# Optimization experiments

Hardware: AMD Instinct MI355X
Metric: run time of the kernel (lower is better)

The kernel has to match this reference:

```python
import jax, jax.numpy as jnp
import numpy as np

TOP_K = 2

def setup_inputs() -> dict:
    key = jax.random.key(0)
    ks = jax.random.split(key, 5)
    N, D, E, H, O = 2048, 1024, 16, 2048, 1024
    s_in = 1.0 / np.sqrt(D)
    s_h = 1.0 / np.sqrt(H)
    return {
        "z": jax.random.normal(ks[0], (N, D), dtype=jnp.float32),
        "router_w": jax.random.normal(ks[1], (E, D), dtype=jnp.float32) * s_in,
        "router_b": jnp.zeros((E,), dtype=jnp.float32),
        "w1": jax.random.normal(ks[2], (E, H, D), dtype=jnp.float32) * s_in,
        "b1": jnp.zeros((E, H), dtype=jnp.float32),
        "w2": jax.random.normal(ks[3], (E, O, H), dtype=jnp.float32) * s_h,
        "b2": jnp.zeros((E, O), dtype=jnp.float32),
    }

def reference(z, router_w, router_b, w1, b1, w2, b2):
    # Router: softmax over experts, then top-k with renormalized weights
    logits = z @ router_w.T + router_b                      # [N, E]
    probs = jax.nn.softmax(logits, axis=-1)                 # [N, E]
    topk_prob, topk_idx = jax.lax.top_k(probs, TOP_K)       # [N, K]
    topk_prob = topk_prob / topk_prob.sum(axis=-1, keepdims=True)

    # Dense all-expert MLP (faithful to original mix(): every expert on every token)
    h = jax.nn.gelu(jnp.einsum('nd,ehd->neh', z, w1) + b1, approximate=False)  # [N, E, H]
    expert_out = jnp.einsum('neh,eoh->neo', h, w2) + b2                        # [N, E, O]

    # Gather top-k expert outputs and combine with routing weights
    picked = jnp.take_along_axis(expert_out, topk_idx[:, :, None], axis=1)     # [N, K, O]
    return (picked * topk_prob[:, :, None]).sum(axis=1)                        # [N, O]
```

## Files before the change

### kernel.cpp

```cpp
#include <hip/hip_runtime.h>
#include <hip/hip_bf16.h>
#include <math.h>

#define N_TOK 2048
#define DIM   1024
#define NE    16
#define NH    2048
#define NO    1024

typedef __attribute__((ext_vector_type(8))) short short8;
typedef __attribute__((ext_vector_type(4))) float f32x4;

__device__ __forceinline__ unsigned short f2bf(float f) {
  union { float f; unsigned u; } v; v.f = f;
  unsigned r = v.u + 0x7FFFu + ((v.u >> 16) & 1u);
  return (unsigned short)(r >> 16);
}

__device__ __forceinline__ short8 pack8(float4 a, float4 b) {
  short8 r;
  r[0] = (short)f2bf(a.x); r[1] = (short)f2bf(a.y);
  r[2] = (short)f2bf(a.z); r[3] = (short)f2bf(a.w);
  r[4] = (short)f2bf(b.x); r[5] = (short)f2bf(b.y);
  r[6] = (short)f2bf(b.z); r[7] = (short)f2bf(b.w);
  return r;
}

__device__ __forceinline__ unsigned pkbf(float x, float y) {
  float2 f; f.x = x; f.y = y;
  __hip_bfloat162 b = __float22bfloat162_rn(f);
  unsigned u; __builtin_memcpy(&u, &b, 4);
  return u;
}
__device__ __forceinline__ short8 cvt8(float4 a, float4 b) {
  union { short8 s; unsigned u[4]; } r;
  r.u[0] = pkbf(a.x, a.y); r.u[1] = pkbf(a.z, a.w);
  r.u[2] = pkbf(b.x, b.y); r.u[3] = pkbf(b.z, b.w);
  return r.s;
}

__device__ __forceinline__ void glds16(const void* g, void* l) {
  __builtin_amdgcn_global_load_lds(
      (const __attribute__((address_space(1))) void*)g,
      (__attribute__((address_space(3))) void*)l, 16, 0, 0);
}

__device__ __forceinline__ void lds_barrier() {
  __builtin_amdgcn_s_waitcnt(0xC07F);
  __builtin_amdgcn_s_barrier();
}

__global__ __launch_bounds__(256) void router_kernel(
    const float* __restrict__ z, const float* __restrict__ rw,
    const float* __restrict__ rb, int* __restrict__ counts,
    int* __restrict__ list, float* __restrict__ tkw) {
  const int n = blockIdx.x;
  const int t = threadIdx.x;
  const int e = t >> 4, sub = t & 15;
  const float* zr = z + (size_t)n * DIM;
  const float* wr = rw + (size_t)e * DIM;
  double acc = 0.0;
#pragma unroll
  for (int i = 0; i < 16; ++i) {
    const int d = i * 64 + sub * 4;
    const float4 zv = *(const float4*)(zr + d);
    const float4 wv = *(const float4*)(wr + d);
    acc += (double)zv.x * wv.x + (double)zv.y * wv.y
         + (double)zv.z * wv.z + (double)zv.w * wv.w;
  }
  acc += __shfl_xor(acc, 8, 16);
  acc += __shfl_xor(acc, 4, 16);
  acc += __shfl_xor(acc, 2, 16);
  acc += __shfl_xor(acc, 1, 16);
  __shared__ double logits[NE];
  if (sub == 0) logits[e] = acc + (double)rb[e];
  __syncthreads();
  if (t == 0) {
    int i0 = -1, i1 = -1; double v0 = -1e300, v1 = -1e300;
    for (int i = 0; i < NE; ++i) {
      const double v = logits[i];
      if (v > v0) { v1 = v0; i1 = i0; v0 = v; i0 = i; }
      else if (v > v1) { v1 = v; i1 = i; }
    }
    const double w0 = 1.0 / (1.0 + exp(v1 - v0));
    tkw[n * 2 + 0] = (float)w0;
    tkw[n * 2 + 1] = (float)(1.0 - w0);
    const int p0 = atomicAdd(&counts[i0], 1); list[i0 * N_TOK + p0] = n * 2;
    const int p1 = atomicAdd(&counts[i1], 1); list[i1 * N_TOK + p1] = n * 2 + 1;
  }
}

__global__ __launch_bounds__(256) void convert_z_kernel(
    const float* __restrict__ z, unsigned short* __restrict__ zbf) {
  const int i = (blockIdx.x * 256 + threadIdx.x) * 8;
  const float4 a = *(const float4*)(z + i);
  const float4 b = *(const float4*)(z + i + 4);
  *(short8*)(zbf + i) = pack8(a, b);
}

#define BM 128
#define BN 128
#define BK 64
#define NNT1 (NH / BN)
#define NNT2 (NO / BN)
#define MT_LEVELS 8

__device__ __forceinline__ void decode_bid(int bid, int nent, int& mt, int& ent) {
  if (bid < 2 * nent) {
    mt = (bid >> 3) & 1;
    ent = (bid >> 4) * 8 + (bid & 7);
  } else {
    const int t2 = bid - 2 * nent;
    mt = 2 + t2 / nent;
    ent = t2 - (mt - 2) * nent;
  }
}

__global__ __launch_bounds__(256, 2) void gemm1_kernel(
    const unsigned short* __restrict__ zbf, const float* __restrict__ w1,
    const float* __restrict__ b1, const int* __restrict__ counts,
    const int* __restrict__ list, unsigned short* __restrict__ h) {
  int mt, ent;
  decode_bid(blockIdx.x, NE * NNT1, mt, ent);
  const int e  = ent >> 4;
  const int nt = ent & 15;
  const int ne = counts[e];
  if (mt * BM >= ne) return;
  const int t = threadIdx.x;

  __shared__ __align__(16) unsigned char As[BM * BK * 2];
  __shared__ __align__(16) unsigned char Bs[BN * BK * 4];
  __shared__ int ent_s[BM];
  if (t < BM) {
    const int idx = mt * BM + t;
    ent_s[t] = (idx < ne) ? list[e * N_TOK + idx] : -1;
  }
  __syncthreads();

  const int lane = t & 63, w = t >> 6;
  const unsigned short* aP[4];
  const float* bP[8];
  unsigned char *aL[4], *bL[8];
  {
    const int l3 = lane >> 3, c7 = lane & 7;
#pragma unroll
    for (int p = 0; p < 4; ++p) {
      const int CI = w + 4 * p;
      const int R = 8 * CI + l3;
      const int c = c7 ^ (R & 7);
      const int en = ent_s[R];
      aP[p] = zbf + (size_t)(en >= 0 ? (en >> 1) : 0) * DIM + c * 8;
      aL[p] = As + CI * 1024;
    }
    const int l4 = lane >> 4, c15 = lane & 15;
    const float* bbase = w1 + ((size_t)e * NH + (size_t)nt * BN) * DIM;
#pragma unroll
    for (int q = 0; q < 8; ++q) {
      const int CI = w + 4 * q;
      const int R = 4 * CI + l4;
      const int c = c15 ^ (R & 15);
      bP[q] = bbase + (size_t)R * DIM + c * 4;
      bL[q] = Bs + CI * 1024;
    }
  }

  const int wm = (w & 1) * 64, wn = (w >> 1) * 64;
  const int l15 = lane & 15, quad = lane >> 4;

  f32x4 acc[4][4];
#pragma unroll
  for (int i = 0; i < 4; ++i)
#pragma unroll
    for (int j = 0; j < 4; ++j) acc[i][j] = (f32x4){0.f, 0.f, 0.f, 0.f};

  for (int k0 = 0; k0 < DIM; k0 += BK) {
#pragma unroll
    for (int p = 0; p < 4; ++p) glds16(aP[p] + k0, aL[p]);
#pragma unroll
    for (int q = 0; q < 8; ++q) glds16(bP[q] + k0, bL[q]);
    __syncthreads();
#pragma unroll
    for (int kk = 0; kk < BK; kk += 32) {
      short8 af[4], bfr[4];
#pragma unroll
      for (int i = 0; i < 4; ++i) {
        const int R = wm + i * 16 + l15;
        const int c0 = (kk >> 3) + quad;
        af[i] = *(const short8*)(As + R * 128 + ((c0 ^ (R & 7)) << 4));
      }
#pragma unroll
      for (int j = 0; j < 4; ++j) {
        const int R = wn + j * 16 + l15;
        const int c0 = (kk >> 2) + 2 * quad;
        const float4 f0 = *(const float4*)(Bs + R * 256 + ((c0 ^ (R & 15)) << 4));
        const float4 f1 = *(const float4*)(Bs + R * 256 + (((c0 + 1) ^ (R & 15)) << 4));
        bfr[j] = cvt8(f0, f1);
      }
#pragma unroll
      for (int i = 0; i < 4; ++i)
#pragma unroll
        for (int j = 0; j < 4; ++j)
          acc[i][j] = __builtin_amdgcn_mfma_f32_16x16x32_bf16(af[i], bfr[j], acc[i][j], 0, 0, 0);
    }
    lds_barrier();
  }

  const int r4 = quad * 4;
#pragma unroll
  for (int i = 0; i < 4; ++i) {
#pragma unroll
    for (int reg = 0; reg < 4; ++reg) {
      const int row = wm + i * 16 + r4 + reg;
      const int en = ent_s[row];
      if (en < 0) continue;
      unsigned short* hrow = h + (size_t)en * NH;
#pragma unroll
      for (int j = 0; j < 4; ++j) {
        const int col = nt * BN + wn + j * 16 + l15;
        float v = acc[i][j][reg] + b1[e * NH + col];
        v = 0.5f * v * (1.0f + erff(v * 0.70710678118654752f));
        hrow[col] = f2bf(v);
      }
    }
  }
}

__global__ __launch_bounds__(256, 2) void gemm2_kernel(
    const unsigned short* __restrict__ h, const float* __restrict__ w2,
    const float* __restrict__ b2, const int* __restrict__ counts,
    const int* __restrict__ list, float* __restrict__ contrib) {
  int mt, ent;
  decode_bid(blockIdx.x, NE * NNT2, mt, ent);
  const int e  = ent >> 3;
  const int nt = ent & 7;
  const int ne = counts[e];
  if (mt * BM >= ne) return;
  const int t = threadIdx.x;

  __shared__ __align__(16) unsigned char As[BM * BK * 2];
  __shared__ __align__(16) unsigned char Bs[BN * BK * 4];
  __shared__ int ent_s[BM];
  if (t < BM) {
    const int idx = mt * BM + t;
    ent_s[t] = (idx < ne) ? list[e * N_TOK + idx] : -1;
  }
  __syncthreads();

  const int lane = t & 63, w = t >> 6;
  const unsigned short* aP[4];
  const float* bP[8];
  unsigned char *aL[4], *bL[8];
  {
    const int l3 = lane >> 3, c7 = lane & 7;
#pragma unroll
    for (int p = 0; p < 4; ++p) {
      const int CI = w + 4 * p;
      const int R = 8 * CI + l3;
      const int c = c7 ^ (R & 7);
      const int en = ent_s[R];
      aP[p] = h + (size_t)(en >= 0 ? en : 0) * NH + c * 8;
      aL[p] = As + CI * 1024;
    }
    const int l4 = lane >> 4, c15 = lane & 15;
    const float* bbase = w2 + ((size_t)e * NO + (size_t)nt * BN) * NH;
#pragma unroll
    for (int q = 0; q < 8; ++q) {
      const int CI = w + 4 * q;
      const int R = 4 * CI + l4;
      const int c = c15 ^ (R & 15);
      bP[q] = bbase + (size_t)R * NH + c * 4;
      bL[q] = Bs + CI * 1024;
    }
  }

  const int wm = (w & 1) * 64, wn = (w >> 1) * 64;
  const int l15 = lane & 15, quad = lane >> 4;

  f32x4 acc[4][4];
#pragma unroll
  for (int i = 0; i < 4; ++i)
#pragma unroll
    for (int j = 0; j < 4; ++j) acc[i][j] = (f32x4){0.f, 0.f, 0.f, 0.f};

  for (int k0 = 0; k0 < NH; k0 += BK) {
#pragma unroll
    for (int p = 0; p < 4; ++p) glds16(aP[p] + k0, aL[p]);
#pragma unroll
    for (int q = 0; q < 8; ++q) glds16(bP[q] + k0, bL[q]);
    __syncthreads();
#pragma unroll
    for (int kk = 0; kk < BK; kk += 32) {
      short8 af[4], bfr[4];
#pragma unroll
      for (int i = 0; i < 4; ++i) {
        const int R = wm + i * 16 + l15;
        const int c0 = (kk >> 3) + quad;
        af[i] = *(const short8*)(As + R * 128 + ((c0 ^ (R & 7)) << 4));
      }
#pragma unroll
      for (int j = 0; j < 4; ++j) {
        const int R = wn + j * 16 + l15;
        const int c0 = (kk >> 2) + 2 * quad;
        const float4 f0 = *(const float4*)(Bs + R * 256 + ((c0 ^ (R & 15)) << 4));
        const float4 f1 = *(const float4*)(Bs + R * 256 + (((c0 + 1) ^ (R & 15)) << 4));
        bfr[j] = cvt8(f0, f1);
      }
#pragma unroll
      for (int i = 0; i < 4; ++i)
#pragma unroll
        for (int j = 0; j < 4; ++j)
          acc[i][j] = __builtin_amdgcn_mfma_f32_16x16x32_bf16(af[i], bfr[j], acc[i][j], 0, 0, 0);
    }
    lds_barrier();
  }

  const int r4 = quad * 4;
#pragma unroll
  for (int i = 0; i < 4; ++i) {
#pragma unroll
    for (int reg = 0; reg < 4; ++reg) {
      const int row = wm + i * 16 + r4 + reg;
      const int en = ent_s[row];
      if (en < 0) continue;
      float* crow = contrib + (size_t)en * NO;
#pragma unroll
      for (int j = 0; j < 4; ++j) {
        const int col = nt * BN + wn + j * 16 + l15;
        crow[col] = acc[i][j][reg] + b2[e * NO + col];
      }
    }
  }
}

__global__ __launch_bounds__(256) void combine_kernel(
    const float* __restrict__ contrib, const float* __restrict__ tkw,
    float* __restrict__ out) {
  const int gid = blockIdx.x * 256 + threadIdx.x;
  const int n = gid >> 8;
  const int c = (gid & 255) * 4;
  const float w0 = tkw[n * 2], w1 = tkw[n * 2 + 1];
  const float4 a = *(const float4*)(contrib + (size_t)(n * 2) * NO + c);
  const float4 b = *(const float4*)(contrib + (size_t)(n * 2 + 1) * NO + c);
  float4 o;
  o.x = w0 * a.x + w1 * b.x; o.y = w0 * a.y + w1 * b.y;
  o.z = w0 * a.z + w1 * b.z; o.w = w0 * a.w + w1 * b.w;
  *(float4*)(out + (size_t)n * NO + c) = o;
}

extern "C" void kernel_launch(void* const* d_in, const int* in_sizes, int n_in,
                              void* d_out, int out_size, void* d_ws, size_t ws_size,
                              hipStream_t stream) {
  const float* z  = (const float*)d_in[0];
  const float* rw = (const float*)d_in[1];
  const float* rb = (const float*)d_in[2];
  const float* w1 = (const float*)d_in[3];
  const float* b1 = (const float*)d_in[4];
  const float* w2 = (const float*)d_in[5];
  const float* b2 = (const float*)d_in[6];
  float* out = (float*)d_out;

  char* ws = (char*)d_ws;
  int*   counts = (int*)ws;
  int*   list   = (int*)(ws + 256);
  float* tkw    = (float*)(ws + 256 + 131072);
  unsigned short* zbf = (unsigned short*)(ws + 262144);
  unsigned short* h = (unsigned short*)(ws + 262144 + 4194304);
  float* contrib = (float*)(ws + 262144 + 4194304 + 16777216);

  hipMemsetAsync(counts, 0, NE * sizeof(int), stream);
  convert_z_kernel<<<(N_TOK * DIM / 8) / 256, 256, 0, stream>>>(z, zbf);
  router_kernel<<<N_TOK, 256, 0, stream>>>(z, rw, rb, counts, list, tkw);
  gemm1_kernel<<<MT_LEVELS * NE * NNT1, 256, 0, stream>>>(zbf, w1, b1, counts, list, h);
  gemm2_kernel<<<MT_LEVELS * NE * NNT2, 256, 0, stream>>>(h, w2, b2, counts, list, contrib);
  combine_kernel<<<(N_TOK * (NO / 4)) / 256, 256, 0, stream>>>(contrib, tkw, out);
}
```

Baseline: 424.8 us.

## Double-buffer GEMM tiles and convert weights to bf16 before LDS store

```diff
diff --git a/kernel.cpp b/kernel.cpp
--- a/kernel.cpp
+++ b/kernel.cpp
@@ -43,11 +43,6 @@
   __builtin_amdgcn_global_load_lds(
       (const __attribute__((address_space(1))) void*)g,
       (__attribute__((address_space(3))) void*)l, 16, 0, 0);
-}
-
-__device__ __forceinline__ void lds_barrier() {
-  __builtin_amdgcn_s_waitcnt(0xC07F);
-  __builtin_amdgcn_s_barrier();
 }
 
 __global__ __launch_bounds__(256) void router_kernel(
@@ -104,6 +99,10 @@
 #define NNT1 (NH / BN)
 #define NNT2 (NO / BN)
 #define MT_LEVELS 8
+#define NT1 (DIM / BK)
+#define NT2 (NH / BK)
+#define ASZ (BM * BK * 2)
+#define BSZ (BN * BK * 2)
 
 __device__ __forceinline__ void decode_bid(int bid, int nent, int& mt, int& ent) {
   if (bid < 2 * nent) {
@@ -128,8 +127,8 @@
   if (mt * BM >= ne) return;
   const int t = threadIdx.x;
 
-  __shared__ __align__(16) unsigned char As[BM * BK * 2];
-  __shared__ __align__(16) unsigned char Bs[BN * BK * 4];
+  __shared__ __align__(16) unsigned char As[2 * ASZ];
+  __shared__ __align__(16) unsigned char Bs[2 * BSZ];
   __shared__ int ent_s[BM];
   if (t < BM) {
     const int idx = mt * BM + t;
@@ -139,8 +138,7 @@
 
   const int lane = t & 63, w = t >> 6;
   const unsigned short* aP[4];
-  const float* bP[8];
-  unsigned char *aL[4], *bL[8];
+  unsigned char* aL[4];
   {
     const int l3 = lane >> 3, c7 = lane & 7;
 #pragma unroll
@@ -152,17 +150,14 @@
       aP[p] = zbf + (size_t)(en >= 0 ? (en >> 1) : 0) * DIM + c * 8;
       aL[p] = As + CI * 1024;
     }
-    const int l4 = lane >> 4, c15 = lane & 15;
-    const float* bbase = w1 + ((size_t)e * NH + (size_t)nt * BN) * DIM;
-#pragma unroll
-    for (int q = 0; q < 8; ++q) {
-      const int CI = w + 4 * q;
-      const int R = 4 * CI + l4;
-      const int c = c15 ^ (R & 15);
-      bP[q] = bbase + (size_t)R * DIM + c * 4;
-      bL[q] = Bs + CI * 1024;
-    }
-  }
+  }
+  const int bR = w * 32 + (lane >> 1);
+  const int bh = lane & 1;
+  const float* bSrc = w1 + ((size_t)e * NH + (size_t)(nt * BN + bR)) * DIM + bh * 32;
+  unsigned char* bW[4];
+#pragma unroll
+  for (int j = 0; j < 4; ++j)
+    bW[j] = Bs + bR * 128 + (((bh * 4 + j) ^ (bR & 7)) << 4);
 
   const int wm = (w & 1) * 64, wn = (w >> 1) * 64;
   const int l15 = lane & 15, quad = lane >> 4;
@@ -173,28 +168,40 @@
 #pragma unroll
     for (int j = 0; j < 4; ++j) acc[i][j] = (f32x4){0.f, 0.f, 0.f, 0.f};
 
-  for (int k0 = 0; k0 < DIM; k0 += BK) {
-#pragma unroll
-    for (int p = 0; p < 4; ++p) glds16(aP[p] + k0, aL[p]);
-#pragma unroll
-    for (int q = 0; q < 8; ++q) glds16(bP[q] + k0, bL[q]);
-    __syncthreads();
+  float4 breg[8];
+#pragma unroll
+  for (int p = 0; p < 4; ++p) glds16(aP[p], aL[p]);
+#pragma unroll
+  for (int j = 0; j < 8; ++j) breg[j] = *(const float4*)(bSrc + j * 4);
+#pragma unroll
+  for (int j = 0; j < 4; ++j)
+    *(short8*)(bW[j]) = cvt8(breg[2 * j], breg[2 * j + 1]);
+  __syncthreads();
+
+  for (int kt = 0; kt < NT1; ++kt) {
+    const int cur = kt & 1, nxt = cur ^ 1;
+    const int k1 = (kt + 1) * BK;
+    if (kt + 1 < NT1) {
+#pragma unroll
+      for (int p = 0; p < 4; ++p) glds16(aP[p] + k1, aL[p] + nxt * ASZ);
+#pragma unroll
+      for (int j = 0; j < 8; ++j) breg[j] = *(const float4*)(bSrc + k1 + j * 4);
+    }
+    const unsigned char* Ac = As + cur * ASZ;
+    const unsigned char* Bc = Bs + cur * BSZ;
 #pragma unroll
     for (int kk = 0; kk < BK; kk += 32) {
       short8 af[4], bfr[4];
+      const int c0 = (kk >> 3) + quad;
 #pragma unroll
       for (int i = 0; i < 4; ++i) {
         const int R = wm + i * 16 + l15;
-        const int c0 = (kk >> 3) + quad;
-        af[i] = *(const short8*)(As + R * 128 + ((c0 ^ (R & 7)) << 4));
+        af[i] = *(const short8*)(Ac + R * 128 + ((c0 ^ (R & 7)) << 4));
       }
 #pragma unroll
       for (int j = 0; j < 4; ++j) {
         const int R = wn + j * 16 + l15;
-        const int c0 = (kk >> 2) + 2 * quad;
-        const float4 f0 = *(const float4*)(Bs + R * 256 + ((c0 ^ (R & 15)) << 4));
-        const float4 f1 = *(const float4*)(Bs + R * 256 + (((c0 + 1) ^ (R & 15)) << 4));
-        bfr[j] = cvt8(f0, f1);
+        bfr[j] = *(const short8*)(Bc + R * 128 + ((c0 ^ (R & 7)) << 4));
       }
 #pragma unroll
       for (int i = 0; i < 4; ++i)
@@ -202,7 +209,12 @@
         for (int j = 0; j < 4; ++j)
           acc[i][j] = __builtin_amdgcn_mfma_f32_16x16x32_bf16(af[i], bfr[j], acc[i][j], 0, 0, 0);
     }
-    lds_barrier();
+    if (kt + 1 < NT1) {
+#pragma unroll
+      for (int j = 0; j < 4; ++j)
+        *(short8*)(bW[j] + nxt * BSZ) = cvt8(breg[2 * j], breg[2 * j + 1]);
+      __syncthreads();
+    }
   }
 
   const int r4 = quad * 4;
@@ -237,8 +249,8 @@
   if (mt * BM >= ne) return;
   const int t = threadIdx.x;
 
-  __shared__ __align__(16) unsigned char As[BM * BK * 2];
-  __shared__ __align__(16) unsigned char Bs[BN * BK * 4];
+  __shared__ __align__(16) unsigned char As[2 * ASZ];
+  __shared__ __align__(16) unsigned char Bs[2 * BSZ];
   __shared__ int ent_s[BM];
   if (t < BM) {
     const int idx = mt * BM + t;
@@ -248,8 +260,7 @@
 
   const int lane = t & 63, w = t >> 6;
   const unsigned short* aP[4];
-  const float* bP[8];
-  unsigned char *aL[4], *bL[8];
+  unsigned char* aL[4];
   {
     const int l3 = lane >> 3, c7 = lane & 7;
 #pragma unroll
@@ -261,17 +272,14 @@
       aP[p] = h + (size_t)(en >= 0 ? en : 0) * NH + c * 8;
       aL[p] = As + CI * 1024;
     }
-    const int l4 = lane >> 4, c15 = lane & 15;
-    const float* bbase = w2 + ((size_t)e * NO + (size_t)nt * BN) * NH;
-#pragma unroll
-    for (int q = 0; q < 8; ++q) {
-      const int CI = w + 4 * q;
-      const int R = 4 * CI + l4;
-      const int c = c15 ^ (R & 15);
-      bP[q] = bbase + (size_t)R * NH + c * 4;
-      bL[q] = Bs + CI * 1024;
-    }
-  }
+  }
+  const int bR = w * 32 + (lane >> 1);
+  const int bh = lane & 1;
+  const float* bSrc = w2 + ((size_t)e * NO + (size_t)(nt * BN + bR)) * NH + bh * 32;
+  unsigned char* bW[4];
+#pragma unroll
+  for (int j = 0; j < 4; ++j)
+    bW[j] = Bs + bR * 128 + (((bh * 4 + j) ^ (bR & 7)) << 4);
 
   const int wm = (w & 1) * 64, wn = (w >> 1) * 64;
   const int l15 = lane & 15, quad = lane >> 4;
@@ -282,28 +290,40 @@
 #pragma unroll
     for (int j = 0; j < 4; ++j) acc[i][j] = (f32x4){0.f, 0.f, 0.f, 0.f};
 
-  for (int k0 = 0; k0 < NH; k0 += BK) {
-#pragma unroll
-    for (int p = 0; p < 4; ++p) glds16(aP[p] + k0, aL[p]);
-#pragma unroll
-    for (int q = 0; q < 8; ++q) glds16(bP[q] + k0, bL[q]);
-    __syncthreads();
+  float4 breg[8];
+#pragma unroll
+  for (int p = 0; p < 4; ++p) glds16(aP[p], aL[p]);
+#pragma unroll
+  for (int j = 0; j < 8; ++j) breg[j] = *(const float4*)(bSrc + j * 4);
+#pragma unroll
+  for (int j = 0; j < 4; ++j)
+    *(short8*)(bW[j]) = cvt8(breg[2 * j], breg[2 * j + 1]);
+  __syncthreads();
+
+  for (int kt = 0; kt < NT2; ++kt) {
+    const int cur = kt & 1, nxt = cur ^ 1;
+    const int k1 = (kt + 1) * BK;
+    if (kt + 1 < NT2) {
+#pragma unroll
+      for (int p = 0; p < 4; ++p) glds16(aP[p] + k1, aL[p] + nxt * ASZ);
+#pragma unroll
+      for (int j = 0; j < 8; ++j) breg[j] = *(const float4*)(bSrc + k1 + j * 4);
+    }
+    const unsigned char* Ac = As + cur * ASZ;
+    const unsigned char* Bc = Bs + cur * BSZ;
 #pragma unroll
     for (int kk = 0; kk < BK; kk += 32) {
       short8 af[4], bfr[4];
+      const int c0 = (kk >> 3) + quad;
 #pragma unroll
       for (int i = 0; i < 4; ++i) {
         const int R = wm + i * 16 + l15;
-        const int c0 = (kk >> 3) + quad;
-        af[i] = *(const short8*)(As + R * 128 + ((c0 ^ (R & 7)) << 4));
+        af[i] = *(const short8*)(Ac + R * 128 + ((c0 ^ (R & 7)) << 4));
       }
 #pragma unroll
       for (int j = 0; j < 4; ++j) {
         const int R = wn + j * 16 + l15;
-        const int c0 = (kk >> 2) + 2 * quad;
-        const float4 f0 = *(const float4*)(Bs + R * 256 + ((c0 ^ (R & 15)) << 4));
-        const float4 f1 = *(const float4*)(Bs + R * 256 + (((c0 + 1) ^ (R & 15)) << 4));
-        bfr[j] = cvt8(f0, f1);
+        bfr[j] = *(const short8*)(Bc + R * 128 + ((c0 ^ (R & 7)) << 4));
       }
 #pragma unroll
       for (int i = 0; i < 4; ++i)
@@ -311,7 +331,12 @@
         for (int j = 0; j < 4; ++j)
           acc[i][j] = __builtin_amdgcn_mfma_f32_16x16x32_bf16(af[i], bfr[j], acc[i][j], 0, 0, 0);
     }
-    lds_barrier();
+    if (kt + 1 < NT2) {
+#pragma unroll
+      for (int j = 0; j < 4; ++j)
+        *(short8*)(bW[j] + nxt * BSZ) = cvt8(breg[2 * j], breg[2 * j + 1]);
+      __syncthreads();
+    }
   }
 
   const int r4 = quad * 4;
```

New measurement: 500.6 us. 1.18x slower.

## Shrink MoE GEMM tiles, remap blocks per XCD, fuse combine via atomics

Applied to the files above, without the earlier changes.

```diff
diff --git a/kernel.cpp b/kernel.cpp
--- a/kernel.cpp
+++ b/kernel.cpp
@@ -98,38 +98,34 @@
   *(short8*)(zbf + i) = pack8(a, b);
 }
 
-#define BM 128
-#define BN 128
+#define BM 64
 #define BK 64
-#define NNT1 (NH / BN)
-#define NNT2 (NO / BN)
-#define MT_LEVELS 8
-
-__device__ __forceinline__ void decode_bid(int bid, int nent, int& mt, int& ent) {
-  if (bid < 2 * nent) {
-    mt = (bid >> 3) & 1;
-    ent = (bid >> 4) * 8 + (bid & 7);
-  } else {
-    const int t2 = bid - 2 * nent;
-    mt = 2 + t2 / nent;
-    ent = t2 - (mt - 2) * nent;
-  }
-}
-
-__global__ __launch_bounds__(256, 2) void gemm1_kernel(
+#define BN1 128
+#define BN2 64
+#define NT1 (DIM / BK)
+#define NT2 (NH / BK)
+#define MT_LEVELS 16
+#define GRID_G 4096
+
+__device__ __forceinline__ void decode_bid_xcd(int bid, int& mt, int& e, int& nt) {
+  const int slot = bid >> 3;
+  e = (bid & 7) + ((slot & 1) << 3);
+  mt = (slot >> 1) & 15;
+  nt = slot >> 5;
+}
+
+__global__ __launch_bounds__(256, 3) void gemm1_kernel(
     const unsigned short* __restrict__ zbf, const float* __restrict__ w1,
     const float* __restrict__ b1, const int* __restrict__ counts,
     const int* __restrict__ list, unsigned short* __restrict__ h) {
-  int mt, ent;
-  decode_bid(blockIdx.x, NE * NNT1, mt, ent);
-  const int e  = ent >> 4;
-  const int nt = ent & 15;
+  int mt, e, nt;
+  decode_bid_xcd(blockIdx.x, mt, e, nt);
   const int ne = counts[e];
   if (mt * BM >= ne) return;
   const int t = threadIdx.x;
 
   __shared__ __align__(16) unsigned char As[BM * BK * 2];
-  __shared__ __align__(16) unsigned char Bs[BN * BK * 4];
+  __shared__ __align__(16) unsigned char Bs[BN1 * BK * 4];
   __shared__ int ent_s[BM];
   if (t < BM) {
     const int idx = mt * BM + t;
@@ -138,13 +134,13 @@
   __syncthreads();
 
   const int lane = t & 63, w = t >> 6;
-  const unsigned short* aP[4];
+  const unsigned short* aP[2];
   const float* bP[8];
-  unsigned char *aL[4], *bL[8];
+  unsigned char *aL[2], *bL[8];
   {
     const int l3 = lane >> 3, c7 = lane & 7;
 #pragma unroll
-    for (int p = 0; p < 4; ++p) {
+    for (int p = 0; p < 2; ++p) {
       const int CI = w + 4 * p;
       const int R = 8 * CI + l3;
       const int c = c7 ^ (R & 7);
@@ -153,7 +149,7 @@
       aL[p] = As + CI * 1024;
     }
     const int l4 = lane >> 4, c15 = lane & 15;
-    const float* bbase = w1 + ((size_t)e * NH + (size_t)nt * BN) * DIM;
+    const float* bbase = w1 + ((size_t)e * NH + (size_t)nt * BN1) * DIM;
 #pragma unroll
     for (int q = 0; q < 8; ++q) {
       const int CI = w + 4 * q;
@@ -164,26 +160,26 @@
     }
   }
 
-  const int wm = (w & 1) * 64, wn = (w >> 1) * 64;
+  const int wm = (w & 1) * 32, wn = (w >> 1) * 64;
   const int l15 = lane & 15, quad = lane >> 4;
 
-  f32x4 acc[4][4];
-#pragma unroll
-  for (int i = 0; i < 4; ++i)
+  f32x4 acc[2][4];
+#pragma unroll
+  for (int i = 0; i < 2; ++i)
 #pragma unroll
     for (int j = 0; j < 4; ++j) acc[i][j] = (f32x4){0.f, 0.f, 0.f, 0.f};
 
   for (int k0 = 0; k0 < DIM; k0 += BK) {
 #pragma unroll
-    for (int p = 0; p < 4; ++p) glds16(aP[p] + k0, aL[p]);
+    for (int p = 0; p < 2; ++p) glds16(aP[p] + k0, aL[p]);
 #pragma unroll
     for (int q = 0; q < 8; ++q) glds16(bP[q] + k0, bL[q]);
     __syncthreads();
 #pragma unroll
     for (int kk = 0; kk < BK; kk += 32) {
-      short8 af[4], bfr[4];
-#pragma unroll
-      for (int i = 0; i < 4; ++i) {
+      short8 af[2], bfr[4];
+#pragma unroll
+      for (int i = 0; i < 2; ++i) {
         const int R = wm + i * 16 + l15;
         const int c0 = (kk >> 3) + quad;
         af[i] = *(const short8*)(As + R * 128 + ((c0 ^ (R & 7)) << 4));
@@ -197,7 +193,7 @@
         bfr[j] = cvt8(f0, f1);
       }
 #pragma unroll
-      for (int i = 0; i < 4; ++i)
+      for (int i = 0; i < 2; ++i)
 #pragma unroll
         for (int j = 0; j < 4; ++j)
           acc[i][j] = __builtin_amdgcn_mfma_f32_16x16x32_bf16(af[i], bfr[j], acc[i][j], 0, 0, 0);
@@ -207,7 +203,7 @@
 
   const int r4 = quad * 4;
 #pragma unroll
-  for (int i = 0; i < 4; ++i) {
+  for (int i = 0; i < 2; ++i) {
 #pragma unroll
     for (int reg = 0; reg < 4; ++reg) {
       const int row = wm + i * 16 + r4 + reg;
@@ -216,7 +212,7 @@
       unsigned short* hrow = h + (size_t)en * NH;
 #pragma unroll
       for (int j = 0; j < 4; ++j) {
-        const int col = nt * BN + wn + j * 16 + l15;
+        const int col = nt * BN1 + wn + j * 16 + l15;
         float v = acc[i][j][reg] + b1[e * NH + col];
         v = 0.5f * v * (1.0f + erff(v * 0.70710678118654752f));
         hrow[col] = f2bf(v);
@@ -225,20 +221,19 @@
   }
 }
 
-__global__ __launch_bounds__(256, 2) void gemm2_kernel(
+__global__ __launch_bounds__(256, 4) void gemm2_kernel(
     const unsigned short* __restrict__ h, const float* __restrict__ w2,
     const float* __restrict__ b2, const int* __restrict__ counts,
-    const int* __restrict__ list, float* __restrict__ contrib) {
-  int mt, ent;
-  decode_bid(blockIdx.x, NE * NNT2, mt, ent);
-  const int e  = ent >> 3;
-  const int nt = ent & 7;
+    const int* __restrict__ list, const float* __restrict__ tkw,
+    float* __restrict__ out) {
+  int mt, e, nt;
+  decode_bid_xcd(blockIdx.x, mt, e, nt);
   const int ne = counts[e];
   if (mt * BM >= ne) return;
   const int t = threadIdx.x;
 
   __shared__ __align__(16) unsigned char As[BM * BK * 2];
-  __shared__ __align__(16) unsigned char Bs[BN * BK * 4];
+  __shared__ __align__(16) unsigned char Bs[BN2 * BK * 4];
   __shared__ int ent_s[BM];
   if (t < BM) {
     const int idx = mt * BM + t;
@@ -247,13 +242,13 @@
   __syncthreads();
 
   const int lane = t & 63, w = t >> 6;
-  const unsigned short* aP[4];
-  const float* bP[8];
-  unsigned char *aL[4], *bL[8];
+  const unsigned short* aP[2];
+  const float* bP[4];
+  unsigned char *aL[2], *bL[4];
   {
     const int l3 = lane >> 3, c7 = lane & 7;
 #pragma unroll
-    for (int p = 0; p < 4; ++p) {
+    for (int p = 0; p < 2; ++p) {
       const int CI = w + 4 * p;
       const int R = 8 * CI + l3;
       const int c = c7 ^ (R & 7);
@@ -262,9 +257,9 @@
       aL[p] = As + CI * 1024;
     }
     const int l4 = lane >> 4, c15 = lane & 15;
-    const float* bbase = w2 + ((size_t)e * NO + (size_t)nt * BN) * NH;
-#pragma unroll
-    for (int q = 0; q < 8; ++q) {
+    const float* bbase = w2 + ((size_t)e * NO + (size_t)nt * BN2) * NH;
+#pragma unroll
+    for (int q = 0; q < 4; ++q) {
       const int CI = w + 4 * q;
       const int R = 4 * CI + l4;
       const int c = c15 ^ (R & 15);
@@ -273,32 +268,32 @@
     }
   }
 
-  const int wm = (w & 1) * 64, wn = (w >> 1) * 64;
+  const int wm = (w & 1) * 32, wn = (w >> 1) * 32;
   const int l15 = lane & 15, quad = lane >> 4;
 
-  f32x4 acc[4][4];
-#pragma unroll
-  for (int i = 0; i < 4; ++i)
-#pragma unroll
-    for (int j = 0; j < 4; ++j) acc[i][j] = (f32x4){0.f, 0.f, 0.f, 0.f};
+  f32x4 acc[2][2];
+#pragma unroll
+  for (int i = 0; i < 2; ++i)
+#pragma unroll
+    for (int j = 0; j < 2; ++j) acc[i][j] = (f32x4){0.f, 0.f, 0.f, 0.f};
 
   for (int k0 = 0; k0 < NH; k0 += BK) {
 #pragma unroll
-    for (int p = 0; p < 4; ++p) glds16(aP[p] + k0, aL[p]);
-#pragma unroll
-    for (int q = 0; q < 8; ++q) glds16(bP[q] + k0, bL[q]);
+    for (int p = 0; p < 2; ++p) glds16(aP[p] + k0, aL[p]);
+#pragma unroll
+    for (int q = 0; q < 4; ++q) glds16(bP[q] + k0, bL[q]);
     __syncthreads();
 #pragma unroll
     for (int kk = 0; kk < BK; kk += 32) {
-      short8 af[4], bfr[4];
-#pragma unroll
-      for (int i = 0; i < 4; ++i) {
+      short8 af[2], bfr[2];
+#pragma unroll
+      for (int i = 0; i < 2; ++i) {
         const int R = wm + i * 16 + l15;
         const int c0 = (kk >> 3) + quad;
         af[i] = *(const short8*)(As + R * 128 + ((c0 ^ (R & 7)) << 4));
       }
 #pragma unroll
-      for (int j = 0; j < 4; ++j) {
+      for (int j = 0; j < 2; ++j) {
         const int R = wn + j * 16 + l15;
         const int c0 = (kk >> 2) + 2 * quad;
         const float4 f0 = *(const float4*)(Bs + R * 256 + ((c0 ^ (R & 15)) << 4));
@@ -306,9 +301,9 @@
         bfr[j] = cvt8(f0, f1);
       }
 #pragma unroll
-      for (int i = 0; i < 4; ++i)
-#pragma unroll
-        for (int j = 0; j < 4; ++j)
+      for (int i = 0; i < 2; ++i)
+#pragma unroll
+        for (int j = 0; j < 2; ++j)
           acc[i][j] = __builtin_amdgcn_mfma_f32_16x16x32_bf16(af[i], bfr[j], acc[i][j], 0, 0, 0);
     }
     lds_barrier();
@@ -316,35 +311,21 @@
 
   const int r4 = quad * 4;
 #pragma unroll
-  for (int i = 0; i < 4; ++i) {
+  for (int i = 0; i < 2; ++i) {
 #pragma unroll
     for (int reg = 0; reg < 4; ++reg) {
       const int row = wm + i * 16 + r4 + reg;
       const int en = ent_s[row];
       if (en < 0) continue;
-      float* crow = contrib + (size_t)en * NO;
-#pragma unroll
-      for (int j = 0; j < 4; ++j) {
-        const int col = nt * BN + wn + j * 16 + l15;
-        crow[col] = acc[i][j][reg] + b2[e * NO + col];
-      }
-    }
-  }
-}
-
-__global__ __launch_bounds__(256) void combine_kernel(
-    const float* __restrict__ contrib, const float* __restrict__ tkw,
-    float* __restrict__ out) {
-  const int gid = blockIdx.x * 256 + threadIdx.x;
-  const int n = gid >> 8;
-  const int c = (gid & 255) * 4;
-  const float w0 = tkw[n * 2], w1 = tkw[n * 2 + 1];
-  const float4 a = *(const float4*)(contrib + (size_t)(n * 2) * NO + c);
-  const float4 b = *(const float4*)(contrib + (size_t)(n * 2 + 1) * NO + c);
-  float4 o;
-  o.x = w0 * a.x + w1 * b.x; o.y = w0 * a.y + w1 * b.y;
-  o.z = w0 * a.z + w1 * b.z; o.w = w0 * a.w + w1 * b.w;
-  *(float4*)(out + (size_t)n * NO + c) = o;
+      const float wgt = tkw[en];
+      float* orow = out + (size_t)(en >> 1) * NO;
+#pragma unroll
+      for (int j = 0; j < 2; ++j) {
+        const int col = nt * BN2 + wn + j * 16 + l15;
+        atomicAdd(&orow[col], wgt * (acc[i][j][reg] + b2[e * NO + col]));
+      }
+    }
+  }
 }
 
 extern "C" void kernel_launch(void* const* d_in, const int* in_sizes, int n_in,
@@ -365,12 +346,11 @@
   float* tkw    = (float*)(ws + 256 + 131072);
   unsigned short* zbf = (unsigned short*)(ws + 262144);
   unsigned short* h = (unsigned short*)(ws + 262144 + 4194304);
-  float* contrib = (float*)(ws + 262144 + 4194304 + 16777216);
 
   hipMemsetAsync(counts, 0, NE * sizeof(int), stream);
+  hipMemsetAsync(out, 0, (size_t)N_TOK * NO * sizeof(float), stream);
   convert_z_kernel<<<(N_TOK * DIM / 8) / 256, 256, 0, stream>>>(z, zbf);
   router_kernel<<<N_TOK, 256, 0, stream>>>(z, rw, rb, counts, list, tkw);
-  gemm1_kernel<<<MT_LEVELS * NE * NNT1, 256, 0, stream>>>(zbf, w1, b1, counts, list, h);
-  gemm2_kernel<<<MT_LEVELS * NE * NNT2, 256, 0, stream>>>(h, w2, b2, counts, list, contrib);
-  combine_kernel<<<(N_TOK * (NO / 4)) / 256, 256, 0, stream>>>(contrib, tkw, out);
-}
+  gemm1_kernel<<<GRID_G, 256, 0, stream>>>(zbf, w1, b1, counts, list, h);
+  gemm2_kernel<<<GRID_G, 256, 0, stream>>>(h, w2, b2, counts, list, tkw, out);
+}
```

Measured after the change: 478.5 us. 1.13x slower.

## Pre-convert expert weights to bf16 and use double-buffered direct-to-LDS GEMMs

Applied to the files above, without the earlier changes.

```diff
diff --git a/kernel.cpp b/kernel.cpp
--- a/kernel.cpp
+++ b/kernel.cpp
@@ -98,6 +98,233 @@
   *(short8*)(zbf + i) = pack8(a, b);
 }
 
+__global__ __launch_bounds__(256) void convert_w_kernel(
+    const float* __restrict__ src, unsigned short* __restrict__ dst) {
+  const size_t i = ((size_t)blockIdx.x * 256 + threadIdx.x) * 8;
+  const float4 a = *(const float4*)(src + i);
+  const float4 b = *(const float4*)(src + i + 4);
+  *(short8*)(dst + i) = cvt8(a, b);
+}
+
+#define BMF 128
+#define BKF 64
+#define ASZF (BMF * BKF * 2)
+
+__global__ __launch_bounds__(256, 2) void gemm1_fast(
+    const unsigned short* __restrict__ zbf, const unsigned short* __restrict__ w1b,
+    const float* __restrict__ b1, const int* __restrict__ counts,
+    const int* __restrict__ list, unsigned short* __restrict__ h) {
+  const int bid = blockIdx.x;
+  const int slot = bid >> 3;
+  const int e  = (bid & 7) | ((slot & 1) << 3);
+  const int mt = (slot >> 1) & 7;
+  const int nt = slot >> 4;
+  const int ne = counts[e];
+  if (mt * BMF >= ne) return;
+  const int t = threadIdx.x;
+
+  __shared__ __align__(16) unsigned char As[2 * ASZF];
+  __shared__ __align__(16) unsigned char Bs[2 * ASZF];
+  __shared__ int ent_s[BMF];
+  if (t < BMF) {
+    const int idx = mt * BMF + t;
+    ent_s[t] = (idx < ne) ? list[e * N_TOK + idx] : -1;
+  }
+  __syncthreads();
+
+  const int lane = t & 63, w = t >> 6;
+  const unsigned short *aP[4], *bP[4];
+  unsigned char *aL[4], *bL[4];
+  {
+    const int l3 = lane >> 3, c7 = lane & 7;
+    const unsigned short* bbase = w1b + ((size_t)e * NH + (size_t)nt * 128) * DIM;
+#pragma unroll
+    for (int p = 0; p < 4; ++p) {
+      const int CI = w + 4 * p;
+      const int R = 8 * CI + l3;
+      const int c = c7 ^ (R & 7);
+      const int en = ent_s[R];
+      aP[p] = zbf + (size_t)(en >= 0 ? (en >> 1) : 0) * DIM + c * 8;
+      aL[p] = As + CI * 1024;
+      bP[p] = bbase + (size_t)R * DIM + c * 8;
+      bL[p] = Bs + CI * 1024;
+    }
+  }
+  const int wm = (w & 1) * 64, wn = (w >> 1) * 64;
+  const int l15 = lane & 15, quad = lane >> 4;
+
+  f32x4 acc[4][4];
+#pragma unroll
+  for (int i = 0; i < 4; ++i)
+#pragma unroll
+    for (int j = 0; j < 4; ++j) acc[i][j] = (f32x4){0.f, 0.f, 0.f, 0.f};
+
+#pragma unroll
+  for (int p = 0; p < 4; ++p) { glds16(aP[p], aL[p]); glds16(bP[p], bL[p]); }
+  __syncthreads();
+
+  for (int kt = 0; kt < 16; ++kt) {
+    const int cur = kt & 1, nxt = cur ^ 1;
+    if (kt + 1 < 16) {
+      const int k1 = (kt + 1) * BKF;
+#pragma unroll
+      for (int p = 0; p < 4; ++p) {
+        glds16(aP[p] + k1, aL[p] + nxt * ASZF);
+        glds16(bP[p] + k1, bL[p] + nxt * ASZF);
+      }
+    }
+    const unsigned char* Ac = As + cur * ASZF;
+    const unsigned char* Bc = Bs + cur * ASZF;
+#pragma unroll
+    for (int kk = 0; kk < BKF; kk += 32) {
+      short8 af[4], bfr[4];
+      const int c0 = (kk >> 3) + quad;
+#pragma unroll
+      for (int i = 0; i < 4; ++i) {
+        const int Ra = wm + i * 16 + l15;
+        af[i] = *(const short8*)(Ac + Ra * 128 + ((c0 ^ (Ra & 7)) << 4));
+        const int Rb = wn + i * 16 + l15;
+        bfr[i] = *(const short8*)(Bc + Rb * 128 + ((c0 ^ (Rb & 7)) << 4));
+      }
+#pragma unroll
+      for (int i = 0; i < 4; ++i)
+#pragma unroll
+        for (int j = 0; j < 4; ++j)
+          acc[i][j] = __builtin_amdgcn_mfma_f32_16x16x32_bf16(af[i], bfr[j], acc[i][j], 0, 0, 0);
+    }
+    __syncthreads();
+  }
+
+  const int r4 = quad * 4;
+#pragma unroll
+  for (int i = 0; i < 4; ++i) {
+#pragma unroll
+    for (int reg = 0; reg < 4; ++reg) {
+      const int row = wm + i * 16 + r4 + reg;
+      const int en = ent_s[row];
+      if (en < 0) continue;
+      unsigned short* hrow = h + (size_t)en * NH;
+#pragma unroll
+      for (int j = 0; j < 4; ++j) {
+        const int col = nt * 128 + wn + j * 16 + l15;
+        float v = acc[i][j][reg] + b1[e * NH + col];
+        v = 0.5f * v * (1.0f + erff(v * 0.70710678118654752f));
+        hrow[col] = f2bf(v);
+      }
+    }
+  }
+}
+
+__global__ __launch_bounds__(256, 2) void gemm2_fast(
+    const unsigned short* __restrict__ h, const unsigned short* __restrict__ w2b,
+    const float* __restrict__ b2, const int* __restrict__ counts,
+    const int* __restrict__ list, const float* __restrict__ tkw,
+    float* __restrict__ out) {
+  const int bid = blockIdx.x;
+  const int slot = bid >> 3;
+  const int e  = (bid & 7) | ((slot & 1) << 3);
+  const int mt = (slot >> 1) & 7;
+  const int rest = slot >> 4;
+  const int nt = rest & 7;
+  const int ks = rest >> 3;
+  const int ne = counts[e];
+  if (mt * BMF >= ne) return;
+  const int t = threadIdx.x;
+
+  __shared__ __align__(16) unsigned char As[2 * ASZF];
+  __shared__ __align__(16) unsigned char Bs[2 * ASZF];
+  __shared__ int ent_s[BMF];
+  if (t < BMF) {
+    const int idx = mt * BMF + t;
+    ent_s[t] = (idx < ne) ? list[e * N_TOK + idx] : -1;
+  }
+  __syncthreads();
+
+  const int lane = t & 63, w = t >> 6;
+  const int kbase = ks * (NH / 2);
+  const unsigned short *aP[4], *bP[4];
+  unsigned char *aL[4], *bL[4];
+  {
+    const int l3 = lane >> 3, c7 = lane & 7;
+    const unsigned short* bbase = w2b + ((size_t)e * NO + (size_t)nt * 128) * NH + kbase;
+#pragma unroll
+    for (int p = 0; p < 4; ++p) {
+      const int CI = w + 4 * p;
+      const int R = 8 * CI + l3;
+      const int c = c7 ^ (R & 7);
+      const int en = ent_s[R];
+      aP[p] = h + (size_t)(en >= 0 ? en : 0) * NH + kbase + c * 8;
+      aL[p] = As + CI * 1024;
+      bP[p] = bbase + (size_t)R * NH + c * 8;
+      bL[p] = Bs + CI * 1024;
+    }
+  }
+  const int wm = (w & 1) * 64, wn = (w >> 1) * 64;
+  const int l15 = lane & 15, quad = lane >> 4;
+
+  f32x4 acc[4][4];
+#pragma unroll
+  for (int i = 0; i < 4; ++i)
+#pragma unroll
+    for (int j = 0; j < 4; ++j) acc[i][j] = (f32x4){0.f, 0.f, 0.f, 0.f};
+
+#pragma unroll
+  for (int p = 0; p < 4; ++p) { glds16(aP[p], aL[p]); glds16(bP[p], bL[p]); }
+  __syncthreads();
+
+  for (int kt = 0; kt < 16; ++kt) {
+    const int cur = kt & 1, nxt = cur ^ 1;
+    if (kt + 1 < 16) {
+      const int k1 = (kt + 1) * BKF;
+#pragma unroll
+      for (int p = 0; p < 4; ++p) {
+        glds16(aP[p] + k1, aL[p] + nxt * ASZF);
+        glds16(bP[p] + k1, bL[p] + nxt * ASZF);
+      }
+    }
+    const unsigned char* Ac = As + cur * ASZF;
+    const unsigned char* Bc = Bs + cur * ASZF;
+#pragma unroll
+    for (int kk = 0; kk < BKF; kk += 32) {
+      short8 af[4], bfr[4];
+      const int c0 = (kk >> 3) + quad;
+#pragma unroll
+      for (int i = 0; i < 4; ++i) {
+        const int Ra = wm + i * 16 + l15;
+        af[i] = *(const short8*)(Ac + Ra * 128 + ((c0 ^ (Ra & 7)) << 4));
+        const int Rb = wn + i * 16 + l15;
+        bfr[i] = *(const short8*)(Bc + Rb * 128 + ((c0 ^ (Rb & 7)) << 4));
+      }
+#pragma unroll
+      for (int i = 0; i < 4; ++i)
+#pragma unroll
+        for (int j = 0; j < 4; ++j)
+          acc[i][j] = __builtin_amdgcn_mfma_f32_16x16x32_bf16(af[i], bfr[j], acc[i][j], 0, 0, 0);
+    }
+    __syncthreads();
+  }
+
+  const int r4 = quad * 4;
+#pragma unroll
+  for (int i = 0; i < 4; ++i) {
+#pragma unroll
+    for (int reg = 0; reg < 4; ++reg) {
+      const int row = wm + i * 16 + r4 + reg;
+      const int en = ent_s[row];
+      if (en < 0) continue;
+      const float wgt = tkw[en];
+      float* orow = out + (size_t)(en >> 1) * NO;
+#pragma unroll
+      for (int j = 0; j < 4; ++j) {
+        const int col = nt * 128 + wn + j * 16 + l15;
+        float v = wgt * acc[i][j][reg];
+        if (ks == 0) v += wgt * b2[e * NO + col];
+        atomicAdd(&orow[col], v);
+      }
+    }
+  }
+}
+
 #define BM 128
 #define BN 128
 #define BK 64
@@ -105,7 +332,7 @@
 #define NNT2 (NO / BN)
 #define MT_LEVELS 8
 
-__device__ __forceinline__ void decode_bid(int bid, int nent, int& mt, int& ent) {
+__device__ __forceinline__ void decode_bid_fb(int bid, int nent, int& mt, int& ent) {
   if (bid < 2 * nent) {
     mt = (bid >> 3) & 1;
     ent = (bid >> 4) * 8 + (bid & 7);
@@ -116,12 +343,12 @@
   }
 }
 
-__global__ __launch_bounds__(256, 2) void gemm1_kernel(
+__global__ __launch_bounds__(256, 2) void gemm1_fb(
     const unsigned short* __restrict__ zbf, const float* __restrict__ w1,
     const float* __restrict__ b1, const int* __restrict__ counts,
     const int* __restrict__ list, unsigned short* __restrict__ h) {
   int mt, ent;
-  decode_bid(blockIdx.x, NE * NNT1, mt, ent);
+  decode_bid_fb(blockIdx.x, NE * NNT1, mt, ent);
   const int e  = ent >> 4;
   const int nt = ent & 15;
   const int ne = counts[e];
@@ -225,12 +452,12 @@
   }
 }
 
-__global__ __launch_bounds__(256, 2) void gemm2_kernel(
+__global__ __launch_bounds__(256, 2) void gemm2_fb(
     const unsigned short* __restrict__ h, const float* __restrict__ w2,
     const float* __restrict__ b2, const int* __restrict__ counts,
     const int* __restrict__ list, float* __restrict__ contrib) {
   int mt, ent;
-  decode_bid(blockIdx.x, NE * NNT2, mt, ent);
+  decode_bid_fb(blockIdx.x, NE * NNT2, mt, ent);
   const int e  = ent >> 3;
   const int nt = ent & 7;
   const int ne = counts[e];
@@ -365,12 +592,28 @@
   float* tkw    = (float*)(ws + 256 + 131072);
   unsigned short* zbf = (unsigned short*)(ws + 262144);
   unsigned short* h = (unsigned short*)(ws + 262144 + 4194304);
-  float* contrib = (float*)(ws + 262144 + 4194304 + 16777216);
+
+  const size_t base = 262144 + 4194304 + 16777216;
+  const size_t w1b_sz = (size_t)NE * NH * DIM * 2;
+  const size_t w2b_sz = (size_t)NE * NO * NH * 2;
+  const size_t need_fast = base + w1b_sz + w2b_sz;
 
   hipMemsetAsync(counts, 0, NE * sizeof(int), stream);
   convert_z_kernel<<<(N_TOK * DIM / 8) / 256, 256, 0, stream>>>(z, zbf);
   router_kernel<<<N_TOK, 256, 0, stream>>>(z, rw, rb, counts, list, tkw);
-  gemm1_kernel<<<MT_LEVELS * NE * NNT1, 256, 0, stream>>>(zbf, w1, b1, counts, list, h);
-  gemm2_kernel<<<MT_LEVELS * NE * NNT2, 256, 0, stream>>>(h, w2, b2, counts, list, contrib);
-  combine_kernel<<<(N_TOK * (NO / 4)) / 256, 256, 0, stream>>>(contrib, tkw, out);
-}
+
+  if (ws_size >= need_fast) {
+    unsigned short* w1b = (unsigned short*)(ws + base);
+    unsigned short* w2b = (unsigned short*)(ws + base + w1b_sz);
+    hipMemsetAsync(out, 0, (size_t)N_TOK * NO * sizeof(float), stream);
+    convert_w_kernel<<<(NE * NH * DIM / 8) / 256, 256, 0, stream>>>(w1, w1b);
+    convert_w_kernel<<<(NE * NO * NH / 8) / 256, 256, 0, stream>>>(w2, w2b);
+    gemm1_fast<<<2048, 256, 0, stream>>>(zbf, w1b, b1, counts, list, h);
+    gemm2_fast<<<2048, 256, 0, stream>>>(h, w2b, b2, counts, list, tkw, out);
+  } else {
+    float* contrib = (float*)(ws + base);
+    gemm1_fb<<<MT_LEVELS * NE * NNT1, 256, 0, stream>>>(zbf, w1, b1, counts, list, h);
+    gemm2_fb<<<MT_LEVELS * NE * NNT2, 256, 0, stream>>>(h, w2, b2, counts, list, contrib);
+    combine_kernel<<<(N_TOK * (NO / 4)) / 256, 256, 0, stream>>>(contrib, tkw, out);
+  }
+}
```

Measured after the change: 534.7 us. 25.9% more time.
